# Performance work log

Measured on AMD Instinct MI355X. Metric: run time of the kernel, lower is better.

## Reference

```python
import jax, jax.numpy as jnp
import numpy as np

B, T1, T2, D, O = 8, 64, 128, 512, 512

def setup_inputs() -> dict:
    key = jax.random.key(0)
    k1, k2, k3 = jax.random.split(key, 3)
    X = jax.random.normal(k1, (B, T1, T2, D), dtype=jnp.float32)
    W = jax.random.normal(k2, (D, O), dtype=jnp.float32) * (1.0 / np.sqrt(D))
    b = jax.random.normal(k3, (O,), dtype=jnp.float32) * 0.01
    return {"X": X, "W": W, "b": b}

def reference(X, W, b):
    # Original serializes this via nested K.rnn scans over time1/time2, but the
    # math is a single per-position dense + bias + tanh activation.
    # btsd,do->btso
    return jnp.tanh(jnp.einsum("btsd,do->btso", X, W) + b)
```

## Files before the change

### kernel.cpp

```cpp
#include <hip/hip_runtime.h>
#include <stdint.h>


typedef short bf16x8 __attribute__((ext_vector_type(8)));
typedef float f32x16 __attribute__((ext_vector_type(16)));

#define KTOT 512
#define NTOT 512
#define WT_BYTES   524288ull
#define WS_NEEDED  WT_BYTES

typedef __attribute__((address_space(3))) uint8_t lds8;
typedef __attribute__((address_space(1))) const uint8_t glb8;

__device__ __forceinline__ uint32_t pk2(float a, float b) {
  uint16_t lo = __builtin_bit_cast(uint16_t, (__bf16)a);
  uint16_t hi = __builtin_bit_cast(uint16_t, (__bf16)b);
  return (uint32_t)lo | ((uint32_t)hi << 16);
}

__device__ __forceinline__ float fast_tanh(float z) {
  float t = __builtin_amdgcn_exp2f(z * 2.8853900817779268f);
  return 1.0f - 2.0f * __builtin_amdgcn_rcpf(t + 1.0f);
}

__device__ __forceinline__ int swz4(int r) { return ((r >> 1) ^ (r >> 3)) & 3; }

__global__ __launch_bounds__(256)
void cvtW_kernel(const float* __restrict__ W, uint8_t* __restrict__ Wt) {
  const int c    = blockIdx.x * 256 + threadIdx.x;
  const int j    = c & 3;
  const int r    = (c >> 2) & 127;
  const int tile = c >> 9;
  const int s    = tile & 15;
  const int bn   = tile >> 4;
  const int n    = bn * 128 + r;
  const int k0   = s * 32 + j * 8;
  float e[8];
#pragma unroll
  for (int i = 0; i < 8; ++i) e[i] = W[(size_t)(k0 + i) * NTOT + n];
  uint4 v = make_uint4(pk2(e[0], e[1]), pk2(e[2], e[3]),
                       pk2(e[4], e[5]), pk2(e[6], e[7]));
  *(uint4*)(Wt + ((size_t)tile << 13) + (r << 6) + ((j ^ swz4(r)) << 4)) = v;
}

__global__ __launch_bounds__(256, 4)
void hotdd_fused(const float* __restrict__ X, const uint8_t* __restrict__ Wt,
                 const float* __restrict__ Bv, float* __restrict__ Y) {
  __shared__ uint8_t Ab0[8192], Ab1[8192], Bb0[8192], Bb1[8192];

  const int d  = blockIdx.x;
  const int bm = ((d >> 5) << 3) | (d & 7);
  const int bn = (d >> 3) & 3;

  const int tid  = threadIdx.x;
  const int lane = tid & 63;
  const int wv   = tid >> 6;
  const int wr   = (wv >> 1) * 64;
  const int wc   = (wv & 1) * 64;
  const int lo5  = lane & 31;
  const int hi1  = lane >> 5;

  const int arow  = wv * 32 + (lane >> 1);
  const int ahalf = lane & 1;
  const float* pA = X + (size_t)(bm * 128 + arow) * KTOT + ahalf * 16;
  const int ak  = swz4(arow);
  const int aw0 = arow * 64 + ((((ahalf << 1) | 0) ^ ak) << 4);
  const int aw1 = arow * 64 + ((((ahalf << 1) | 1) ^ ak) << 4);

  const uint8_t* pB = Wt + ((size_t)(bn * 16) << 13) + wv * 2048 + lane * 16;
  uint8_t* Bd0 = Bb0 + wv * 2048;
  uint8_t* Bd1 = Bb1 + wv * 2048;

  const int rA0 = wr + lo5, rA1 = rA0 + 32;
  const int rB0 = wc + lo5, rB1 = rB0 + 32;
  const int oA0 = rA0 * 64, oA1 = rA1 * 64;
  const int oB0 = rB0 * 64, oB1 = rB1 * 64;
  const int kA0 = swz4(rA0), kA1 = swz4(rA1);
  const int kB0 = swz4(rB0), kB1 = swz4(rB1);

  float4 pa0, pa1, pa2, pa3;
  f32x16 acc00 = {}, acc01 = {}, acc10 = {}, acc11 = {};

#define BGLDS(BD, S) do {                                                     \
    const uint8_t* bs_ = pB + ((size_t)(S) << 13);                            \
    __builtin_amdgcn_global_load_lds((glb8*)bs_, (lds8*)(BD), 16, 0, 0);      \
    __builtin_amdgcn_global_load_lds((glb8*)(bs_ + 1024),                     \
                                     (lds8*)((BD) + 1024), 16, 0, 0);         \
  } while (0)

#define LOADA(S) do {                                                         \
    const float* ap_ = pA + (S) * 32;                                         \
    pa0 = *(const float4*)(ap_ + 0);  pa1 = *(const float4*)(ap_ + 4);        \
    pa2 = *(const float4*)(ap_ + 8);  pa3 = *(const float4*)(ap_ + 12);       \
  } while (0)

#define CVTA(AB) do {                                                         \
    *(uint4*)((AB) + aw0) = make_uint4(pk2(pa0.x, pa0.y), pk2(pa0.z, pa0.w),  \
                                       pk2(pa1.x, pa1.y), pk2(pa1.z, pa1.w)); \
    *(uint4*)((AB) + aw1) = make_uint4(pk2(pa2.x, pa2.y), pk2(pa2.z, pa2.w),  \
                                       pk2(pa3.x, pa3.y), pk2(pa3.z, pa3.w)); \
  } while (0)

#define MFMA_STEP(AB, BB) do {                                                \
    _Pragma("unroll")                                                         \
    for (int kk = 0; kk < 2; ++kk) {                                          \
      const int c_ = (kk << 1) | hi1;                                         \
      bf16x8 fa0 = *(const bf16x8*)((AB) + oA0 + ((c_ ^ kA0) << 4));          \
      bf16x8 fa1 = *(const bf16x8*)((AB) + oA1 + ((c_ ^ kA1) << 4));          \
      bf16x8 fb0 = *(const bf16x8*)((BB) + oB0 + ((c_ ^ kB0) << 4));          \
      bf16x8 fb1 = *(const bf16x8*)((BB) + oB1 + ((c_ ^ kB1) << 4));          \
      acc00 = __builtin_amdgcn_mfma_f32_32x32x16_bf16(fa0, fb0, acc00, 0,0,0);\
      acc01 = __builtin_amdgcn_mfma_f32_32x32x16_bf16(fa0, fb1, acc01, 0,0,0);\
      acc10 = __builtin_amdgcn_mfma_f32_32x32x16_bf16(fa1, fb0, acc10, 0,0,0);\
      acc11 = __builtin_amdgcn_mfma_f32_32x32x16_bf16(fa1, fb1, acc11, 0,0,0);\
    }                                                                         \
  } while (0)

#define VMCNT0()  asm volatile("s_waitcnt vmcnt(0)" ::: "memory")
#define LGKM0()   asm volatile("s_waitcnt lgkmcnt(0)" ::: "memory")

  BGLDS(Bd0, 0);
  LOADA(0);
  VMCNT0();
  CVTA(Ab0);
  LGKM0();
  __builtin_amdgcn_s_barrier();

#pragma unroll 1
  for (int t = 0; t < 14; t += 2) {
    BGLDS(Bd1, t + 1);
    LOADA(t + 1);
    MFMA_STEP(Ab0, Bb0);
    VMCNT0();
    CVTA(Ab1);
    LGKM0();
    __builtin_amdgcn_s_barrier();

    BGLDS(Bd0, t + 2);
    LOADA(t + 2);
    MFMA_STEP(Ab1, Bb1);
    VMCNT0();
    CVTA(Ab0);
    LGKM0();
    __builtin_amdgcn_s_barrier();
  }
  BGLDS(Bd1, 15);
  LOADA(15);
  MFMA_STEP(Ab0, Bb0);
  VMCNT0();
  CVTA(Ab1);
  LGKM0();
  __builtin_amdgcn_s_barrier();
  MFMA_STEP(Ab1, Bb1);

  const int gn0 = bn * 128 + wc + lo5;
  const int gn1 = gn0 + 32;
  const float bv0 = Bv[gn0];
  const float bv1 = Bv[gn1];

#define EPI(ACC, MI, GN, BVAL) do {                                           \
    _Pragma("unroll")                                                         \
    for (int r = 0; r < 16; ++r) {                                            \
      const int mloc = wr + (MI) * 32 + (hi1 << 2) + ((r >> 2) << 3) + (r & 3);\
      Y[(size_t)(bm * 128 + mloc) * NTOT + (GN)] = fast_tanh((ACC)[r] + (BVAL));\
    }                                                                         \
  } while (0)

  EPI(acc00, 0, gn0, bv0);
  EPI(acc01, 0, gn1, bv1);
  EPI(acc10, 1, gn0, bv0);
  EPI(acc11, 1, gn1, bv1);
}

struct Regs {
  float4 a0,a1,a2,a3,a4,a5,a6,a7;
  float4 u0,u1,u2,u3;
  float4 v0,v1,v2,v3;
};

__global__ __launch_bounds__(256, 2)
void hotdd_fallback(const float* __restrict__ X, const float* __restrict__ W,
                    const float* __restrict__ Bv, float* __restrict__ Y) {
  __shared__ char Ab[128 * 64 * 2];
  __shared__ char Bb[128 * 64 * 2];
  const int d  = blockIdx.x;
  const int bm = ((d >> 5) << 3) | (d & 7);
  const int bn = (d >> 3) & 3;
  const int tid  = threadIdx.x;
  const int lane = tid & 63;
  const int wv   = tid >> 6;
  const int wr   = (wv >> 1) * 64;
  const int wc   = (wv & 1) * 64;
  const int lo5  = lane & 31;
  const int hi1  = lane >> 5;
  const int rs   = lo5 & 7;
  const int am   = tid >> 1;
  const int ah   = tid & 1;
  const int amz  = am & 7;
  const int abase = am * 128;
  const float* Ag = X + (size_t)(bm * 128 + am) * KTOT + ah * 32;
  const int kp = lo5;
  const int ng = wv * 32 + hi1 * 16;
  const float* Bg = W + (size_t)(2 * kp) * NTOT + bn * 128 + ng;

#define LOADR(R, K0) do {                                                     \
    const float* ap_ = Ag + (K0);                                             \
    R.a0 = *(const float4*)(ap_ +  0); R.a1 = *(const float4*)(ap_ +  4);     \
    R.a2 = *(const float4*)(ap_ +  8); R.a3 = *(const float4*)(ap_ + 12);     \
    R.a4 = *(const float4*)(ap_ + 16); R.a5 = *(const float4*)(ap_ + 20);     \
    R.a6 = *(const float4*)(ap_ + 24); R.a7 = *(const float4*)(ap_ + 28);     \
    const float* bp_ = Bg + (size_t)(K0) * NTOT;                              \
    R.u0 = *(const float4*)(bp_ +  0); R.u1 = *(const float4*)(bp_ +  4);     \
    R.u2 = *(const float4*)(bp_ +  8); R.u3 = *(const float4*)(bp_ + 12);     \
    R.v0 = *(const float4*)(bp_ + NTOT +  0); R.v1 = *(const float4*)(bp_ + NTOT +  4); \
    R.v2 = *(const float4*)(bp_ + NTOT +  8); R.v3 = *(const float4*)(bp_ + NTOT + 12); \
  } while (0)

#define ASTF(R, J, P, Q)                                                      \
    *(uint4*)(Ab + abase + (((((ah << 2) + (J)) ^ amz)) << 4)) =              \
      make_uint4(pk2(R.P.x, R.P.y), pk2(R.P.z, R.P.w),                        \
                 pk2(R.Q.x, R.Q.y), pk2(R.Q.z, R.Q.w));
#define BSTF(R, I, UV, C)                                                     \
    *(uint32_t*)(Bb + (ng + (I)) * 128 + ((kp << 2) ^ (((I) & 7) << 4))) =    \
      pk2(R.u##UV.C, R.v##UV.C);

#define STORERF(R) do {                                                       \
    ASTF(R, 0, a0, a1) ASTF(R, 1, a2, a3) ASTF(R, 2, a4, a5) ASTF(R, 3, a6, a7)\
    BSTF(R, 0, 0, x) BSTF(R, 1, 0, y) BSTF(R, 2, 0, z) BSTF(R, 3, 0, w)       \
    BSTF(R, 4, 1, x) BSTF(R, 5, 1, y) BSTF(R, 6, 1, z) BSTF(R, 7, 1, w)       \
    BSTF(R, 8, 2, x) BSTF(R, 9, 2, y) BSTF(R,10, 2, z) BSTF(R,11, 2, w)       \
    BSTF(R,12, 3, x) BSTF(R,13, 3, y) BSTF(R,14, 3, z) BSTF(R,15, 3, w)       \
  } while (0)

  f32x16 acc00 = {}, acc01 = {}, acc10 = {}, acc11 = {};
  const char* Ard0 = Ab + (wr + lo5) * 128;
  const char* Ard1 = Ard0 + 32 * 128;
  const char* Brd0 = Bb + (wc + lo5) * 128;
  const char* Brd1 = Brd0 + 32 * 128;

#define MFMA_PHASE_F() do {                                                   \
    _Pragma("unroll")                                                         \
    for (int kk = 0; kk < 4; ++kk) {                                          \
      const int sb = ((((kk << 1) | hi1) ^ rs) << 4);                         \
      bf16x8 fa0 = *(const bf16x8*)(Ard0 + sb);                               \
      bf16x8 fa1 = *(const bf16x8*)(Ard1 + sb);                               \
      bf16x8 fb0 = *(const bf16x8*)(Brd0 + sb);                               \
      bf16x8 fb1 = *(const bf16x8*)(Brd1 + sb);                               \
      acc00 = __builtin_amdgcn_mfma_f32_32x32x16_bf16(fa0, fb0, acc00, 0,0,0);\
      acc01 = __builtin_amdgcn_mfma_f32_32x32x16_bf16(fa0, fb1, acc01, 0,0,0);\
      acc10 = __builtin_amdgcn_mfma_f32_32x32x16_bf16(fa1, fb0, acc10, 0,0,0);\
      acc11 = __builtin_amdgcn_mfma_f32_32x32x16_bf16(fa1, fb1, acc11, 0,0,0);\
    }                                                                         \
  } while (0)

  Regs r0, r1;
  LOADR(r0, 0);
#pragma unroll 1
  for (int s = 0; s < 8; s += 2) {
    STORERF(r0);
    __syncthreads();
    LOADR(r1, (s + 1) * 64);
    MFMA_PHASE_F();
    __syncthreads();
    STORERF(r1);
    __syncthreads();
    if (s + 2 < 8) LOADR(r0, (s + 2) * 64);
    MFMA_PHASE_F();
    __syncthreads();
  }

  const int gn0 = bn * 128 + wc + lo5;
  const int gn1 = gn0 + 32;
  const float bv0 = Bv[gn0];
  const float bv1 = Bv[gn1];
  EPI(acc00, 0, gn0, bv0);
  EPI(acc01, 0, gn1, bv1);
  EPI(acc10, 1, gn0, bv0);
  EPI(acc11, 1, gn1, bv1);
}

extern "C" void kernel_launch(void* const* d_in, const int* in_sizes, int n_in,
                              void* d_out, int out_size, void* d_ws, size_t ws_size,
                              hipStream_t stream) {
  (void)in_sizes; (void)n_in; (void)out_size;
  const float* X = (const float*)d_in[0];
  const float* W = (const float*)d_in[1];
  const float* b = (const float*)d_in[2];
  float* Y = (float*)d_out;
  if (ws_size >= WS_NEEDED) {
    uint8_t* Wt = (uint8_t*)d_ws;
    hipLaunchKernelGGL(cvtW_kernel, dim3(128),  dim3(256), 0, stream, W, Wt);
    hipLaunchKernelGGL(hotdd_fused, dim3(2048), dim3(256), 0, stream, X, Wt, b, Y);
  } else {
    hipLaunchKernelGGL(hotdd_fallback, dim3(2048), dim3(256), 0, stream, X, W, b, Y);
  }
}
```

Measured before the change: 84.27 us.

## Prefetch A tiles two stages ahead with register double-buffering and partial vmcnt waits

Splits the A-tile register staging into two register sets so global loads of X run two k-steps ahead of the MFMA consumption. Full vmcnt(0) waits are replaced with counted waits, so B's LDS-direct loads and the next A loads can stay in flight across barriers. Occupancy hint drops from 4 to 3 waves per SIMD to make room for the extra registers. The gain is more memory latency hiding, at the cost of register pressure and fragile manual waitcnt accounting that depends on how the compiler orders instructions.

```diff
diff --git a/kernel.cpp b/kernel.cpp
--- a/kernel.cpp
+++ b/kernel.cpp
@@ -44,7 +44,7 @@
   *(uint4*)(Wt + ((size_t)tile << 13) + (r << 6) + ((j ^ swz4(r)) << 4)) = v;
 }
 
-__global__ __launch_bounds__(256, 4)
+__global__ __launch_bounds__(256, 3)
 void hotdd_fused(const float* __restrict__ X, const uint8_t* __restrict__ Wt,
                  const float* __restrict__ Bv, float* __restrict__ Y) {
   __shared__ uint8_t Ab0[8192], Ab1[8192], Bb0[8192], Bb1[8192];
@@ -79,27 +79,34 @@
   const int kA0 = swz4(rA0), kA1 = swz4(rA1);
   const int kB0 = swz4(rB0), kB1 = swz4(rB1);
 
-  float4 pa0, pa1, pa2, pa3;
+  float4 ra0, ra1, ra2, ra3;
+  float4 rb0, rb1, rb2, rb3;
   f32x16 acc00 = {}, acc01 = {}, acc10 = {}, acc11 = {};
+
+#define SEP() asm volatile("" ::: "memory")
+#define VM(N)  asm volatile("s_waitcnt vmcnt(" #N ")" ::: "memory")
+#define LGKM0() asm volatile("s_waitcnt lgkmcnt(0)" ::: "memory")
 
 #define BGLDS(BD, S) do {                                                     \
     const uint8_t* bs_ = pB + ((size_t)(S) << 13);                            \
     __builtin_amdgcn_global_load_lds((glb8*)bs_, (lds8*)(BD), 16, 0, 0);      \
     __builtin_amdgcn_global_load_lds((glb8*)(bs_ + 1024),                     \
                                      (lds8*)((BD) + 1024), 16, 0, 0);         \
-  } while (0)
-
-#define LOADA(S) do {                                                         \
+    SEP();                                                                    \
+  } while (0)
+
+#define LOADA(R0, R1, R2, R3, S) do {                                         \
     const float* ap_ = pA + (S) * 32;                                         \
-    pa0 = *(const float4*)(ap_ + 0);  pa1 = *(const float4*)(ap_ + 4);        \
-    pa2 = *(const float4*)(ap_ + 8);  pa3 = *(const float4*)(ap_ + 12);       \
-  } while (0)
-
-#define CVTA(AB) do {                                                         \
-    *(uint4*)((AB) + aw0) = make_uint4(pk2(pa0.x, pa0.y), pk2(pa0.z, pa0.w),  \
-                                       pk2(pa1.x, pa1.y), pk2(pa1.z, pa1.w)); \
-    *(uint4*)((AB) + aw1) = make_uint4(pk2(pa2.x, pa2.y), pk2(pa2.z, pa2.w),  \
-                                       pk2(pa3.x, pa3.y), pk2(pa3.z, pa3.w)); \
+    R0 = *(const float4*)(ap_ + 0);  R1 = *(const float4*)(ap_ + 4);          \
+    R2 = *(const float4*)(ap_ + 8);  R3 = *(const float4*)(ap_ + 12);         \
+    SEP();                                                                    \
+  } while (0)
+
+#define CVTA(R0, R1, R2, R3, AB) do {                                         \
+    *(uint4*)((AB) + aw0) = make_uint4(pk2(R0.x, R0.y), pk2(R0.z, R0.w),      \
+                                       pk2(R1.x, R1.y), pk2(R1.z, R1.w));     \
+    *(uint4*)((AB) + aw1) = make_uint4(pk2(R2.x, R2.y), pk2(R2.z, R2.w),      \
+                                       pk2(R3.x, R3.y), pk2(R3.z, R3.w));     \
   } while (0)
 
 #define MFMA_STEP(AB, BB) do {                                                \
@@ -117,40 +124,41 @@
     }                                                                         \
   } while (0)
 
-#define VMCNT0()  asm volatile("s_waitcnt vmcnt(0)" ::: "memory")
-#define LGKM0()   asm volatile("s_waitcnt lgkmcnt(0)" ::: "memory")
-
+  LOADA(ra0, ra1, ra2, ra3, 0);
   BGLDS(Bd0, 0);
-  LOADA(0);
-  VMCNT0();
-  CVTA(Ab0);
+  LOADA(rb0, rb1, rb2, rb3, 1);
+  VM(6);
+  CVTA(ra0, ra1, ra2, ra3, Ab0);
   LGKM0();
-  __builtin_amdgcn_s_barrier();
 
 #pragma unroll 1
   for (int t = 0; t < 14; t += 2) {
+    VM(4);
+    __builtin_amdgcn_s_barrier();
     BGLDS(Bd1, t + 1);
-    LOADA(t + 1);
+    LOADA(ra0, ra1, ra2, ra3, t + 2);
     MFMA_STEP(Ab0, Bb0);
-    VMCNT0();
-    CVTA(Ab1);
+    VM(6);
+    CVTA(rb0, rb1, rb2, rb3, Ab1);
     LGKM0();
+    VM(4);
     __builtin_amdgcn_s_barrier();
-
     BGLDS(Bd0, t + 2);
-    LOADA(t + 2);
+    LOADA(rb0, rb1, rb2, rb3, t + 3);
     MFMA_STEP(Ab1, Bb1);
-    VMCNT0();
-    CVTA(Ab0);
+    VM(6);
+    CVTA(ra0, ra1, ra2, ra3, Ab0);
     LGKM0();
-    __builtin_amdgcn_s_barrier();
   }
+
+  VM(4);
+  __builtin_amdgcn_s_barrier();
   BGLDS(Bd1, 15);
-  LOADA(15);
   MFMA_STEP(Ab0, Bb0);
-  VMCNT0();
-  CVTA(Ab1);
+  VM(2);
+  CVTA(rb0, rb1, rb2, rb3, Ab1);
   LGKM0();
+  VM(0);
   __builtin_amdgcn_s_barrier();
   MFMA_STEP(Ab1, Bb1);
 
```

New measurement: 78.39 us. 7.0% less time.
